# Performance work log

Measured on AMD Instinct MI355X. Metric: run time of the kernel, lower is better.

Reference implementation:

```python
import jax, jax.numpy as jnp
import numpy as np

N = 8192      # number of tree nodes
IN = 1024     # in_dim
M = 1024      # effective mem_dim = 2 * mem_dim_init
K = 8         # max children (complete 8-ary tree)


def _linear_init(key, out_dim, in_dim):
    k1, k2 = jax.random.split(key)
    s = 1.0 / np.sqrt(in_dim)
    w = jax.random.uniform(k1, (out_dim, in_dim), minval=-s, maxval=s, dtype=jnp.float32)
    b = jax.random.uniform(k2, (out_dim,), minval=-s, maxval=s, dtype=jnp.float32)
    return w, b


def setup_inputs() -> dict:
    key = jax.random.key(0)
    ks = jax.random.split(key, 5)
    w_ioux, b_ioux = _linear_init(ks[0], 3 * M, IN)
    w_iouh, b_iouh = _linear_init(ks[1], 3 * M, M)
    w_fx, b_fx = _linear_init(ks[2], M, IN)
    w_fh, b_fh = _linear_init(ks[3], M, M)
    inputs = jax.random.normal(ks[4], (N, IN), dtype=jnp.float32)
    # Complete K-ary tree: children of node p are p*K+1 .. p*K+K (clipped).
    # Pad with index N, which addresses an always-zero dummy row.
    ch = np.full((N, K), N, dtype=np.int32)
    for j in range(K):
        idx = np.arange(N) * K + 1 + j
        valid = idx < N
        ch[valid, j] = idx[valid]
    return dict(inputs=inputs, children=jnp.asarray(ch),
                w_ioux=w_ioux, b_ioux=b_ioux, w_iouh=w_iouh, b_iouh=b_iouh,
                w_fx=w_fx, b_fx=b_fx, w_fh=w_fh, b_fh=b_fh)


def reference(inputs, children, w_ioux, b_ioux, w_iouh, b_iouh, w_fx, b_fx, w_fh, b_fh):
    # Precompute the input-side projections for all nodes at once.
    iou_x = inputs @ w_ioux.T + b_ioux   # [N, 3M]
    fx_x = inputs @ w_fx.T + b_fx        # [N, M]
    h0 = jnp.zeros((N + 1, M), inputs.dtype)  # row N is the zero pad slot
    c0 = jnp.zeros((N + 1, M), inputs.dtype)

    def step(carry, t):
        h_buf, c_buf = carry
        ch = children[t]           # [K] child indices (pad = N -> zero rows)
        ch_h = h_buf[ch]           # [K, M] real child h's
        ch_c = c_buf[ch]           # [K, M] real child c's
        # Faithful to original: for internal nodes child_c/child_h are SWAPPED,
        # so the 'child_h_sum' and f-gate inputs use the real c's, while the
        # forgotten memory (fc) multiplies the real h's. Leaves: all zeros.
        csum = ch_c.sum(0)                                   # [M]
        iou = iou_x[t] + csum @ w_iouh.T + b_iouh            # [3M]
        i_g, o_g, u_g = jnp.split(iou, 3)
        i_g = jax.nn.sigmoid(i_g)
        o_g = jax.nn.sigmoid(o_g)
        u_g = jnp.tanh(u_g)
        f = jax.nn.sigmoid(ch_c @ w_fh.T + b_fh + fx_x[t])   # [K, M]
        c = i_g * u_g + (f * ch_h).sum(0)                    # [M]
        h = o_g * jnp.tanh(c)
        return (h_buf.at[t].set(h), c_buf.at[t].set(c)), None

    # Children always have larger indices than their parent, so processing
    # t = N-1 .. 0 matches the original reverse-BFS (leaves-first) order.
    order = jnp.arange(N - 1, -1, -1)
    (h_buf, c_buf), _ = jax.lax.scan(step, (h0, c0), order)
    root_h = h_buf[0][None, :]   # [1, M]
    root_c = c_buf[0][None, :]   # [1, M]
    return root_h, root_c
```

## Files before the change

kernel.cpp:

```cpp
#include <hip/hip_runtime.h>

typedef __bf16 bf16x8 __attribute__((ext_vector_type(8)));
typedef __attribute__((ext_vector_type(4))) float f4;

#define AS1 __attribute__((address_space(1)))
#define AS3 __attribute__((address_space(3)))

__device__ __forceinline__ unsigned short f2bf(float f) {
    union { float f; unsigned int u; } x; x.f = f;
    return (unsigned short)((x.u + 0x7fffu + ((x.u >> 16) & 1u)) >> 16);
}
__device__ __forceinline__ float bf2f(unsigned short u) {
    union { unsigned int u; float f; } x; x.u = (unsigned int)u << 16;
    return x.f;
}
__device__ __forceinline__ float fsigm(float x) {
    return __builtin_amdgcn_rcpf(1.f + __expf(-x));
}
__device__ __forceinline__ float ftanh(float x) {
    return 1.f - 2.f * __builtin_amdgcn_rcpf(1.f + __expf(2.f * x));
}
__device__ __forceinline__ void gload_lds16(const unsigned short* g, unsigned short* l) {
    __builtin_amdgcn_global_load_lds((const AS1 unsigned int*)g, (AS3 unsigned int*)l, 16, 0, 0);
}
__device__ __forceinline__ void bar() {
    asm volatile("" ::: "memory");
    __builtin_amdgcn_s_barrier();
    asm volatile("" ::: "memory");
}

__global__ void prep_all_k(const float* __restrict__ inputs, const float* __restrict__ w_ioux,
                           const float* __restrict__ w_fx, const float* __restrict__ w_iouh,
                           const float* __restrict__ w_fh,
                           const float* __restrict__ b_ioux, const float* __restrict__ b_iouh,
                           const float* __restrict__ b_fx, const float* __restrict__ b_fh,
                           unsigned short* __restrict__ Xbf, unsigned short* __restrict__ Wiouxbf,
                           unsigned short* __restrict__ Wfxbf, unsigned short* __restrict__ Whbf,
                           unsigned short* __restrict__ Wfhbf,
                           float* __restrict__ bias_iou, float* __restrict__ bias_f,
                           unsigned short* __restrict__ c_bf, unsigned short* __restrict__ h_bf) {
    int b = blockIdx.x;
    if (b < 16384) {
        int idx = b * 256 + threadIdx.x;
        const float* src; unsigned short* dst; int rel;
        if (idx < 2097152)      { src = inputs; dst = Xbf;     rel = idx; }
        else if (idx < 2883584) { src = w_ioux; dst = Wiouxbf; rel = idx - 2097152; }
        else if (idx < 3145728) { src = w_fx;   dst = Wfxbf;   rel = idx - 2883584; }
        else if (idx < 3932160) { src = w_iouh; dst = Whbf;    rel = idx - 3145728; }
        else                    { src = w_fh;   dst = Wfhbf;   rel = idx - 3932160; }
        float4 v = reinterpret_cast<const float4*>(src)[rel];
        ushort4 o; o.x = f2bf(v.x); o.y = f2bf(v.y); o.z = f2bf(v.z); o.w = f2bf(v.w);
        reinterpret_cast<ushort4*>(dst)[rel] = o;
    } else if (b < 16400) {
        int idx = (b - 16384) * 256 + threadIdx.x;
        if (idx < 3072) bias_iou[idx] = b_ioux[idx] + b_iouh[idx];
        else { int j = idx - 3072; bias_f[j] = b_fx[j] + b_fh[j]; }
    } else {
        int j = (b - 16400) * 256 + threadIdx.x;
        size_t o = (size_t)8192 * 1024 + j;
        c_bf[o] = 0; h_bf[o] = 0;
    }
}

__device__ __forceinline__ void stage_half(const unsigned short* __restrict__ G,
                                           int trow0, int kt, unsigned short* lds_region, int tid) {
#pragma unroll
    for (int ii = 0; ii < 2; ++ii) {
        int c = ii * 512 + tid;
        int r = c >> 3, sl = c & 7;
        gload_lds16(G + (size_t)(trow0 + r) * 1024 + kt * 64 + ((sl ^ (r & 7)) * 8),
                    lds_region + c * 8);
    }
}
__device__ __forceinline__ bf16x8 rdfrag(const unsigned short* region, int rowih, int kslot) {
    return *reinterpret_cast<const bf16x8*>(&region[rowih * 64 + ((kslot ^ (rowih & 7)) * 8)]);
}

#define RD_A(AF, REG, FB)                                                        \
    _Pragma("unroll") for (int f_ = 0; f_ < 4; ++f_)                             \
    _Pragma("unroll") for (int s_ = 0; s_ < 2; ++s_)                             \
        (AF)[f_][s_] = rdfrag((REG), ((FB) + f_) * 16 + fr, s_ * 4 + q);
#define RD_B(BQ, REG, GB)                                                        \
    _Pragma("unroll") for (int g_ = 0; g_ < 2; ++g_)                             \
    _Pragma("unroll") for (int s_ = 0; s_ < 2; ++s_)                             \
        (BQ)[g_][s_] = rdfrag((REG), bcol0 + ((GB) + g_) * 16 + fr, s_ * 4 + q);
#define MF16(FB, GB, AF, BQ)                                                     \
    __builtin_amdgcn_s_setprio(1);                                               \
    _Pragma("unroll") for (int s_ = 0; s_ < 2; ++s_)                             \
    _Pragma("unroll") for (int f_ = 0; f_ < 4; ++f_)                             \
    _Pragma("unroll") for (int g_ = 0; g_ < 2; ++g_)                             \
        acc[(FB) + f_][(GB) + g_] = __builtin_amdgcn_mfma_f32_16x16x32_bf16(     \
            (AF)[f_][s_], (BQ)[g_][s_], acc[(FB) + f_][(GB) + g_], 0, 0, 0);     \
    __builtin_amdgcn_s_setprio(0);

__device__ __forceinline__ void gemm256_core(const unsigned short* __restrict__ Am,
                                             const unsigned short* __restrict__ Bm,
                                             int tm, int tn,
                                             unsigned short* ls, f4 acc[8][4]) {
    const int tid = threadIdx.x;
    const int l = tid & 63, w = tid >> 6;
    const int wm = w >> 2, wn = w & 3;
    const int fr = l & 15, q = l >> 4;
    const int bcol0 = (wn & 1) * 64;

    unsigned short* S0 = ls;
    unsigned short* S1 = ls + 32768;
    const unsigned short* Ar0 = S0 + wm * 8192;
    const unsigned short* Br0 = S0 + (2 + (wn >> 1)) * 8192;
    const unsigned short* Ar1 = S1 + wm * 8192;
    const unsigned short* Br1 = S1 + (2 + (wn >> 1)) * 8192;

#pragma unroll
    for (int i = 0; i < 8; ++i)
#pragma unroll
        for (int j = 0; j < 4; ++j) acc[i][j] = (f4){0.f, 0.f, 0.f, 0.f};

    stage_half(Am, tm,       0, S0 + 0 * 8192, tid);
    stage_half(Am, tm + 128, 0, S0 + 1 * 8192, tid);
    stage_half(Bm, tn,       0, S0 + 2 * 8192, tid);
    stage_half(Bm, tn + 128, 0, S0 + 3 * 8192, tid);
    stage_half(Bm, tn,       1, S1 + 2 * 8192, tid);
    stage_half(Bm, tn + 128, 1, S1 + 3 * 8192, tid);
    asm volatile("s_waitcnt vmcnt(4)" ::: "memory");
    bar();

    for (int i = 0; i < 8; ++i) {
        bf16x8 afA[4][2], afB[4][2], bq01[2][2], bq23[2][2];
        RD_A(afA, Ar0, 0)
        RD_B(bq01, Br0, 0)
        stage_half(Am, tm,       2 * i + 1, S1 + 0 * 8192, tid);
        asm volatile("s_waitcnt lgkmcnt(8)" ::: "memory");
        bar();
        MF16(0, 0, afA, bq01)
        bar();
        RD_B(bq23, Br0, 2)
        stage_half(Am, tm + 128, 2 * i + 1, S1 + 1 * 8192, tid);
        bar();
        MF16(0, 2, afA, bq23)
        bar();
        RD_A(afB, Ar0, 4)
        if (i < 7) stage_half(Bm, tn,       2 * i + 2, S0 + 2 * 8192, tid);
        bar();
        MF16(4, 2, afB, bq23)
        bar();
        if (i < 7) {
            stage_half(Bm, tn + 128, 2 * i + 2, S0 + 3 * 8192, tid);
            asm volatile("s_waitcnt vmcnt(4)" ::: "memory");
        } else {
            asm volatile("s_waitcnt vmcnt(0)" ::: "memory");
        }
        bar();
        MF16(4, 0, afB, bq01)
        bar();
        RD_A(afA, Ar1, 0)
        RD_B(bq01, Br1, 0)
        if (i < 7) stage_half(Am, tm,       2 * i + 2, S0 + 0 * 8192, tid);
        asm volatile("s_waitcnt lgkmcnt(8)" ::: "memory");
        bar();
        MF16(0, 0, afA, bq01)
        bar();
        RD_B(bq23, Br1, 2)
        if (i < 7) stage_half(Am, tm + 128, 2 * i + 2, S0 + 1 * 8192, tid);
        bar();
        MF16(0, 2, afA, bq23)
        bar();
        RD_A(afB, Ar1, 4)
        if (i < 7) stage_half(Bm, tn,       2 * i + 3, S1 + 2 * 8192, tid);
        bar();
        MF16(4, 2, afB, bq23)
        bar();
        if (i < 7) {
            stage_half(Bm, tn + 128, 2 * i + 3, S1 + 3 * 8192, tid);
            asm volatile("s_waitcnt vmcnt(4)" ::: "memory");
        } else {
            asm volatile("s_waitcnt vmcnt(0)" ::: "memory");
        }
        bar();
        MF16(4, 0, afB, bq01)
        bar();
    }
}

__global__ __launch_bounds__(512, 2)
void gemm_big_k(const unsigned short* __restrict__ Xbf, const unsigned short* __restrict__ Wioux,
                const unsigned short* __restrict__ Wfx,
                const float* __restrict__ bias_iou, const float* __restrict__ bias_f,
                unsigned short* __restrict__ P_iou, unsigned short* __restrict__ P_f) {
    __shared__ unsigned short ls[65536];
    int b = blockIdx.x;
    b = (b & 7) * 50 + (b >> 3);
    const unsigned short* Bm; unsigned short* Cp; const float* biasp;
    int tm, tn, ldc;
    if (b < 384) {
        int st = b / 24, wt = b % 24;
        tm = ((st >> 2) * 8 + wt / 3) * 256;
        tn = ((st & 3) * 3 + wt % 3) * 256;
        Bm = Wioux; Cp = P_iou; biasp = bias_iou; ldc = 3072;
    } else {
        int bb = b - 384;
        tm = (bb & 3) * 256; tn = (bb >> 2) * 256;
        Bm = Wfx; Cp = P_f; biasp = bias_f; ldc = 1024;
    }
    f4 acc[8][4];
    gemm256_core(Xbf, Bm, tm, tn, ls, acc);

    const int l = threadIdx.x & 63, w = threadIdx.x >> 6;
    const int wm = w >> 2, wn = w & 3;
    const int fr = l & 15, q = l >> 4;
#pragma unroll
    for (int f = 0; f < 8; ++f)
#pragma unroll
        for (int g = 0; g < 4; ++g) {
            int col = tn + wn * 64 + g * 16 + fr;
            float bv = biasp[col];
#pragma unroll
            for (int r = 0; r < 4; ++r) {
                int row = tm + wm * 128 + f * 16 + q * 4 + r;
                Cp[(size_t)row * ldc + col] = f2bf(acc[f][g][r] + bv);
            }
        }
}

__device__ __forceinline__ void gemm_core_db(const unsigned short* __restrict__ A,
                                             const unsigned short* __restrict__ B,
                                             int M, int tile_m, int tile_n, int kb, int nsteps,
                                             unsigned short* lsA, unsigned short* lsB,
                                             f4 acc[4][4]) {
    const int K = 1024;
    const int tid = threadIdx.x;
    const int l = tid & 63, wid = tid >> 6;
    const int wm = wid >> 1, wn = wid & 1;
    const int fr = l & 15, q = l >> 4;

#pragma unroll
    for (int i = 0; i < 4; ++i)
#pragma unroll
        for (int j = 0; j < 4; ++j) acc[i][j] = (f4){0.f, 0.f, 0.f, 0.f};

    const unsigned short* ga[4]; const unsigned short* gb[4];
    unsigned short *la[4], *lb[4];
#pragma unroll
    for (int i = 0; i < 4; ++i) {
        int chunk = i * 256 + tid;
        int row = chunk >> 3, slot = chunk & 7;
        int scol = (slot ^ (row & 7)) * 8;
        ga[i] = A + (size_t)min(tile_m + row, M - 1) * K + kb * 64 + scol;
        gb[i] = B + (size_t)(tile_n + row) * K + kb * 64 + scol;
        la[i] = lsA + chunk * 8;
        lb[i] = lsB + chunk * 8;
    }
#pragma unroll
    for (int i = 0; i < 4; ++i) gload_lds16(ga[i], la[i]);
#pragma unroll
    for (int i = 0; i < 4; ++i) gload_lds16(gb[i], lb[i]);

    int roffA[4], roffB[4];
#pragma unroll
    for (int f = 0; f < 4; ++f) {
        roffA[f] = (wm * 64 + f * 16 + fr) * 64;
        roffB[f] = (wn * 64 + f * 16 + fr) * 64;
    }
    const int sw = fr & 7;
    int cur = 0;
    for (int t = 0; t < nsteps; ++t) {
        if (t < nsteps - 1) {
            int k0 = (t + 1) * 64;
            int nb = (cur ^ 1) * 8192;
#pragma unroll
            for (int i = 0; i < 4; ++i) gload_lds16(ga[i] + k0, la[i] + nb);
#pragma unroll
            for (int i = 0; i < 4; ++i) gload_lds16(gb[i] + k0, lb[i] + nb);
            asm volatile("s_waitcnt vmcnt(8)" ::: "memory");
        } else {
            asm volatile("s_waitcnt vmcnt(0)" ::: "memory");
        }
        __builtin_amdgcn_s_barrier();
        const unsigned short* bA = lsA + cur * 8192;
        const unsigned short* bB = lsB + cur * 8192;
        bf16x8 af[4][2], bq[4][2];
#pragma unroll
        for (int f = 0; f < 4; ++f)
#pragma unroll
            for (int s = 0; s < 2; ++s) {
                int sl = ((s * 4 + q) ^ sw) * 8;
                af[f][s] = *reinterpret_cast<const bf16x8*>(&bA[roffA[f] + sl]);
                bq[f][s] = *reinterpret_cast<const bf16x8*>(&bB[roffB[f] + sl]);
            }
#pragma unroll
        for (int s = 0; s < 2; ++s)
#pragma unroll
            for (int i = 0; i < 4; ++i)
#pragma unroll
                for (int j = 0; j < 4; ++j)
                    acc[i][j] = __builtin_amdgcn_mfma_f32_16x16x32_bf16(af[i][s], bq[j][s], acc[i][j], 0, 0, 0);
        __builtin_amdgcn_s_barrier();
        cur ^= 1;
    }
}

__global__ void leafact_csum_k(const unsigned short* __restrict__ P_iou,
                               unsigned short* __restrict__ h_bf, unsigned short* __restrict__ c_bf,
                               unsigned short* __restrict__ csum_bf) {
    int b = blockIdx.x;
    int j = threadIdx.x * 4;
    if (b < 896) {
        int p = 128 + b;
        float s0 = 0.f, s1 = 0.f, s2 = 0.f, s3 = 0.f;
#pragma unroll
        for (int k = 0; k < 8; ++k) {
            int t = p * 8 + 1 + k;
            const unsigned short* pp = P_iou + (size_t)t * 3072 + j;
            ushort4 pi = *reinterpret_cast<const ushort4*>(pp);
            ushort4 po = *reinterpret_cast<const ushort4*>(pp + 1024);
            ushort4 pu = *reinterpret_cast<const ushort4*>(pp + 2048);
            float c0 = fsigm(bf2f(pi.x)) * ftanh(bf2f(pu.x));
            float c1 = fsigm(bf2f(pi.y)) * ftanh(bf2f(pu.y));
            float c2 = fsigm(bf2f(pi.z)) * ftanh(bf2f(pu.z));
            float c3 = fsigm(bf2f(pi.w)) * ftanh(bf2f(pu.w));
            ushort4 cb, hb;
            cb.x = f2bf(c0); hb.x = f2bf(fsigm(bf2f(po.x)) * ftanh(c0));
            cb.y = f2bf(c1); hb.y = f2bf(fsigm(bf2f(po.y)) * ftanh(c1));
            cb.z = f2bf(c2); hb.z = f2bf(fsigm(bf2f(po.z)) * ftanh(c2));
            cb.w = f2bf(c3); hb.w = f2bf(fsigm(bf2f(po.w)) * ftanh(c3));
            size_t o = (size_t)t * 1024 + j;
            *reinterpret_cast<ushort4*>(c_bf + o) = cb;
            *reinterpret_cast<ushort4*>(h_bf + o) = hb;
            s0 += c0; s1 += c1; s2 += c2; s3 += c3;
        }
        ushort4 sv; sv.x = f2bf(s0); sv.y = f2bf(s1); sv.z = f2bf(s2); sv.w = f2bf(s3);
        *reinterpret_cast<ushort4*>(csum_bf + (size_t)p * 1024 + j) = sv;
    } else {
        const int t = 1024;
        const unsigned short* pp = P_iou + (size_t)t * 3072 + j;
        ushort4 pi = *reinterpret_cast<const ushort4*>(pp);
        ushort4 po = *reinterpret_cast<const ushort4*>(pp + 1024);
        ushort4 pu = *reinterpret_cast<const ushort4*>(pp + 2048);
        float c0 = fsigm(bf2f(pi.x)) * ftanh(bf2f(pu.x));
        float c1 = fsigm(bf2f(pi.y)) * ftanh(bf2f(pu.y));
        float c2 = fsigm(bf2f(pi.z)) * ftanh(bf2f(pu.z));
        float c3 = fsigm(bf2f(pi.w)) * ftanh(bf2f(pu.w));
        ushort4 cb, hb;
        cb.x = f2bf(c0); hb.x = f2bf(fsigm(bf2f(po.x)) * ftanh(c0));
        cb.y = f2bf(c1); hb.y = f2bf(fsigm(bf2f(po.y)) * ftanh(c1));
        cb.z = f2bf(c2); hb.z = f2bf(fsigm(bf2f(po.z)) * ftanh(c2));
        cb.w = f2bf(c3); hb.w = f2bf(fsigm(bf2f(po.w)) * ftanh(c3));
        size_t o = (size_t)t * 1024 + j;
        *reinterpret_cast<ushort4*>(c_bf + o) = cb;
        *reinterpret_cast<ushort4*>(h_bf + o) = hb;
    }
}

__global__ void csum_k(const unsigned short* __restrict__ c_bf, unsigned short* __restrict__ csum_bf,
                       int lo, int n) {
    int w = blockIdx.x * blockDim.x + threadIdx.x;
    if (w >= n * 256) return;
    int tt = w >> 8, j = (w & 255) * 4;
    int t = lo + tt;
    size_t base = (size_t)(t * 8 + 1) * 1024 + j;
    float s0 = 0.f, s1 = 0.f, s2 = 0.f, s3 = 0.f;
#pragma unroll
    for (int k = 0; k < 8; ++k) {
        ushort4 v = *reinterpret_cast<const ushort4*>(c_bf + base + (size_t)k * 1024);
        s0 += bf2f(v.x); s1 += bf2f(v.y); s2 += bf2f(v.z); s3 += bf2f(v.w);
    }
    ushort4 o; o.x = f2bf(s0); o.y = f2bf(s1); o.z = f2bf(s2); o.w = f2bf(s3);
    *reinterpret_cast<ushort4*>(csum_bf + (size_t)t * 1024 + j) = o;
}

__global__ void node_update_k(const unsigned short* __restrict__ P_iou,
                              const unsigned short* __restrict__ P_f,
                              const float* __restrict__ out_iouh, const float* __restrict__ out_f,
                              unsigned short* __restrict__ h_bf, unsigned short* __restrict__ c_bf,
                              float* __restrict__ out, int lo, int n) {
    int w = blockIdx.x * blockDim.x + threadIdx.x;
    if (w >= n * 256) return;
    int tt = w >> 8, j = (w & 255) * 4;
    int t = lo + tt;
    const unsigned short* p = P_iou + (size_t)t * 3072 + j;
    ushort4 pi4 = *reinterpret_cast<const ushort4*>(p);
    ushort4 po4 = *reinterpret_cast<const ushort4*>(p + 1024);
    ushort4 pu4 = *reinterpret_cast<const ushort4*>(p + 2048);
    const float* oi = out_iouh + (size_t)tt * 3072 + j;
    f4 oii = *reinterpret_cast<const f4*>(oi);
    f4 oio = *reinterpret_cast<const f4*>(oi + 1024);
    f4 oiu = *reinterpret_cast<const f4*>(oi + 2048);
    ushort4 pf4 = *reinterpret_cast<const ushort4*>(P_f + (size_t)t * 1024 + j);
    float pf[4] = {bf2f(pf4.x), bf2f(pf4.y), bf2f(pf4.z), bf2f(pf4.w)};
    float a[4], og[4];
    a[0] = fsigm(bf2f(pi4.x) + oii[0]) * ftanh(bf2f(pu4.x) + oiu[0]);
    a[1] = fsigm(bf2f(pi4.y) + oii[1]) * ftanh(bf2f(pu4.y) + oiu[1]);
    a[2] = fsigm(bf2f(pi4.z) + oii[2]) * ftanh(bf2f(pu4.z) + oiu[2]);
    a[3] = fsigm(bf2f(pi4.w) + oii[3]) * ftanh(bf2f(pu4.w) + oiu[3]);
    og[0] = fsigm(bf2f(po4.x) + oio[0]);
    og[1] = fsigm(bf2f(po4.y) + oio[1]);
    og[2] = fsigm(bf2f(po4.z) + oio[2]);
    og[3] = fsigm(bf2f(po4.w) + oio[3]);
#pragma unroll
    for (int k = 0; k < 8; ++k) {
        f4 fo = *reinterpret_cast<const f4*>(out_f + (size_t)(tt * 8 + k) * 1024 + j);
        ushort4 hc = *reinterpret_cast<const ushort4*>(h_bf + (size_t)(t * 8 + 1 + k) * 1024 + j);
        a[0] += fsigm(pf[0] + fo[0]) * bf2f(hc.x);
        a[1] += fsigm(pf[1] + fo[1]) * bf2f(hc.y);
        a[2] += fsigm(pf[2] + fo[2]) * bf2f(hc.z);
        a[3] += fsigm(pf[3] + fo[3]) * bf2f(hc.w);
    }
    float h0 = og[0] * ftanh(a[0]);
    float h1 = og[1] * ftanh(a[1]);
    float h2 = og[2] * ftanh(a[2]);
    float h3 = og[3] * ftanh(a[3]);
    size_t o = (size_t)t * 1024 + j;
    ushort4 cb; cb.x = f2bf(a[0]); cb.y = f2bf(a[1]); cb.z = f2bf(a[2]); cb.w = f2bf(a[3]);
    ushort4 hb; hb.x = f2bf(h0); hb.y = f2bf(h1); hb.z = f2bf(h2); hb.w = f2bf(h3);
    *reinterpret_cast<ushort4*>(c_bf + o) = cb;
    *reinterpret_cast<ushort4*>(h_bf + o) = hb;
    if (t == 0) {
        f4 hv = {h0, h1, h2, h3};
        f4 cv = {a[0], a[1], a[2], a[3]};
        *reinterpret_cast<f4*>(out + j) = hv;
        *reinterpret_cast<f4*>(out + 1024 + j) = cv;
    }
}

struct GDesc {
    const unsigned short* A;
    const unsigned short* B;
    float* C;
    int M;
    int ldc;
    int tiles_n;
    int tiles_total;
};

__global__ __launch_bounds__(256)
void gemm_dual_k(GDesc d0, GDesc d1) {
    __shared__ unsigned short lsA[16384];
    __shared__ unsigned short lsB[16384];
    int b = blockIdx.x;
    GDesc d; int bb;
    if (b < d0.tiles_total) { d = d0; bb = b; }
    else { d = d1; bb = b - d0.tiles_total; }
    const int tile_m = (bb / d.tiles_n) * 128;
    const int tile_n = (bb % d.tiles_n) * 128;
    f4 acc[4][4];
    gemm_core_db(d.A, d.B, d.M, tile_m, tile_n, 0, 16, lsA, lsB, acc);

    const int l = threadIdx.x & 63, wid = threadIdx.x >> 6;
    const int wm = wid >> 1, wn = wid & 1;
    const int fr = l & 15, q = l >> 4;
#pragma unroll
    for (int i = 0; i < 4; ++i)
#pragma unroll
        for (int j = 0; j < 4; ++j) {
            int col = tile_n + wn * 64 + fr + j * 16;
#pragma unroll
            for (int r = 0; r < 4; ++r) {
                int row = tile_m + wm * 64 + q * 4 + i * 16 + r;
                if (row < d.M) d.C[(size_t)row * d.ldc + col] = acc[i][j][r];
            }
        }
}

__global__ __launch_bounds__(256)
void gemm_tail_k(const unsigned short* __restrict__ c_bf,
                 const unsigned short* __restrict__ Whbf, const unsigned short* __restrict__ Wfhbf,
                 float* __restrict__ part_iouh, float* __restrict__ part_f, int lo, int n) {
    __shared__ unsigned short lsA[16384];
    __shared__ unsigned short lsB[16384];
    const int tid = threadIdx.x;
    const int l = tid & 63, wid = tid >> 6;
    const int wm = wid >> 1, wn = wid & 1;
    const int fr = l & 15, q = l >> 4;
    int b = blockIdx.x;
    f4 acc[4][4];
    float* C; int M, ldc, tm, tn;

    if (b < 96) {
        const int split = b & 3, tile = b >> 2;
        M = n; ldc = 3072; tm = 0; tn = tile * 128;
        C = part_iouh + (size_t)split * 64 * 3072;
        for (int e = tid; e < n * 64; e += 256) {
            int r = e >> 6, c4 = e & 63;
            size_t gbase = (size_t)((lo + r) * 8 + 1) * 1024 + split * 256 + c4 * 4;
            float s0 = 0.f, s1 = 0.f, s2 = 0.f, s3 = 0.f;
#pragma unroll
            for (int k = 0; k < 8; ++k) {
                ushort4 v = *reinterpret_cast<const ushort4*>(c_bf + gbase + (size_t)k * 1024);
                s0 += bf2f(v.x); s1 += bf2f(v.y); s2 += bf2f(v.z); s3 += bf2f(v.w);
            }
            ushort4 o; o.x = f2bf(s0); o.y = f2bf(s1); o.z = f2bf(s2); o.w = f2bf(s3);
            int sl8 = c4 >> 1, half = c4 & 1;
            int phys = (sl8 & ~7) | ((sl8 & 7) ^ (r & 7));
            *reinterpret_cast<ushort4*>(&lsA[r * 256 + phys * 8 + half * 4]) = o;
        }
        const unsigned short* gb[4]; unsigned short* lb[4];
#pragma unroll
        for (int i = 0; i < 4; ++i) {
            int chunk = i * 256 + tid;
            int row = chunk >> 3, slot = chunk & 7;
            int scol = (slot ^ (row & 7)) * 8;
            gb[i] = Whbf + (size_t)(tn + row) * 1024 + split * 256 + scol;
            lb[i] = lsB + chunk * 8;
        }
#pragma unroll
        for (int i = 0; i < 4; ++i) gload_lds16(gb[i], lb[i]);
        asm volatile("s_waitcnt lgkmcnt(0)" ::: "memory");
        __builtin_amdgcn_s_barrier();

#pragma unroll
        for (int i2 = 0; i2 < 4; ++i2)
#pragma unroll
            for (int j2 = 0; j2 < 4; ++j2) acc[i2][j2] = (f4){0.f, 0.f, 0.f, 0.f};
        int roffB[4], rA[4];
#pragma unroll
        for (int f = 0; f < 4; ++f) {
            roffB[f] = (wn * 64 + f * 16 + fr) * 64;
            rA[f] = min(wm * 64 + f * 16 + fr, n - 1);
        }
        const int sw = fr & 7;
        int cur = 0;
        for (int t = 0; t < 4; ++t) {
            if (t < 3) {
                int nb = (cur ^ 1) * 8192;
#pragma unroll
                for (int i = 0; i < 4; ++i) gload_lds16(gb[i] + (t + 1) * 64, lb[i] + nb);
                asm volatile("s_waitcnt vmcnt(4)" ::: "memory");
            } else {
                asm volatile("s_waitcnt vmcnt(0)" ::: "memory");
            }
            __builtin_amdgcn_s_barrier();
            const unsigned short* bB = lsB + cur * 8192;
            bf16x8 af[4][2], bq[4][2];
#pragma unroll
            for (int f = 0; f < 4; ++f)
#pragma unroll
                for (int s = 0; s < 2; ++s) {
                    int x = s * 4 + q;
                    af[f][s] = *reinterpret_cast<const bf16x8*>(
                        &lsA[rA[f] * 256 + (t * 8 + (x ^ (rA[f] & 7))) * 8]);
                    bq[f][s] = *reinterpret_cast<const bf16x8*>(&bB[roffB[f] + ((x ^ sw) * 8)]);
                }
// ... 34 lines not shown
                                   const unsigned short* __restrict__ P_f,
                                   const float* __restrict__ part_iouh,
                                   const float* __restrict__ part_f,
                                   unsigned short* __restrict__ h_bf, unsigned short* __restrict__ c_bf,
                                   float* __restrict__ out, int lo, int n) {
    int w = blockIdx.x * blockDim.x + threadIdx.x;
    if (w >= n * 256) return;
    int tt = w >> 8, j = (w & 255) * 4;
    int t = lo + tt;
    f4 oii = {0.f, 0.f, 0.f, 0.f}, oio = oii, oiu = oii;
#pragma unroll
    for (int s = 0; s < 4; ++s) {
        const float* base = part_iouh + (size_t)s * 64 * 3072 + (size_t)tt * 3072 + j;
        oii += *reinterpret_cast<const f4*>(base);
        oio += *reinterpret_cast<const f4*>(base + 1024);
        oiu += *reinterpret_cast<const f4*>(base + 2048);
    }
    const unsigned short* p = P_iou + (size_t)t * 3072 + j;
    ushort4 pi4 = *reinterpret_cast<const ushort4*>(p);
    ushort4 po4 = *reinterpret_cast<const ushort4*>(p + 1024);
    ushort4 pu4 = *reinterpret_cast<const ushort4*>(p + 2048);
    ushort4 pf4 = *reinterpret_cast<const ushort4*>(P_f + (size_t)t * 1024 + j);
    float pf[4] = {bf2f(pf4.x), bf2f(pf4.y), bf2f(pf4.z), bf2f(pf4.w)};
    float a[4], og[4];
    a[0] = fsigm(bf2f(pi4.x) + oii[0]) * ftanh(bf2f(pu4.x) + oiu[0]);
    a[1] = fsigm(bf2f(pi4.y) + oii[1]) * ftanh(bf2f(pu4.y) + oiu[1]);
    a[2] = fsigm(bf2f(pi4.z) + oii[2]) * ftanh(bf2f(pu4.z) + oiu[2]);
    a[3] = fsigm(bf2f(pi4.w) + oii[3]) * ftanh(bf2f(pu4.w) + oiu[3]);
    og[0] = fsigm(bf2f(po4.x) + oio[0]);
    og[1] = fsigm(bf2f(po4.y) + oio[1]);
    og[2] = fsigm(bf2f(po4.z) + oio[2]);
    og[3] = fsigm(bf2f(po4.w) + oio[3]);
#pragma unroll
    for (int k = 0; k < 8; ++k) {
        f4 fo = {0.f, 0.f, 0.f, 0.f};
#pragma unroll
        for (int s = 0; s < 4; ++s)
            fo += *reinterpret_cast<const f4*>(part_f + (size_t)s * 512 * 1024 +
                                               (size_t)(tt * 8 + k) * 1024 + j);
        ushort4 hc = *reinterpret_cast<const ushort4*>(h_bf + (size_t)(t * 8 + 1 + k) * 1024 + j);
        a[0] += fsigm(pf[0] + fo[0]) * bf2f(hc.x);
        a[1] += fsigm(pf[1] + fo[1]) * bf2f(hc.y);
        a[2] += fsigm(pf[2] + fo[2]) * bf2f(hc.z);
        a[3] += fsigm(pf[3] + fo[3]) * bf2f(hc.w);
    }
    float h0 = og[0] * ftanh(a[0]);
    float h1 = og[1] * ftanh(a[1]);
    float h2 = og[2] * ftanh(a[2]);
    float h3 = og[3] * ftanh(a[3]);
    size_t o = (size_t)t * 1024 + j;
    ushort4 cb; cb.x = f2bf(a[0]); cb.y = f2bf(a[1]); cb.z = f2bf(a[2]); cb.w = f2bf(a[3]);
    ushort4 hb; hb.x = f2bf(h0); hb.y = f2bf(h1); hb.z = f2bf(h2); hb.w = f2bf(h3);
    *reinterpret_cast<ushort4*>(c_bf + o) = cb;
    *reinterpret_cast<ushort4*>(h_bf + o) = hb;
    if (t == 0) {
        f4 hv = {h0, h1, h2, h3};
        f4 cv = {a[0], a[1], a[2], a[3]};
        *reinterpret_cast<f4*>(out + j) = hv;
        *reinterpret_cast<f4*>(out + 1024 + j) = cv;
    }
}

extern "C" void kernel_launch(void* const* d_in, const int* in_sizes, int n_in,
                              void* d_out, int out_size, void* d_ws, size_t ws_size,
                              hipStream_t stream) {
    const float* inputs = (const float*)d_in[0];
    const float* w_ioux = (const float*)d_in[2];
    const float* b_ioux = (const float*)d_in[3];
    const float* w_iouh = (const float*)d_in[4];
    const float* b_iouh = (const float*)d_in[5];
    const float* w_fx   = (const float*)d_in[6];
    const float* b_fx   = (const float*)d_in[7];
    const float* w_fh   = (const float*)d_in[8];
    const float* b_fh   = (const float*)d_in[9];
    float* out = (float*)d_out;

    char* ws = (char*)d_ws;
    size_t off = 0;
    auto alloc = [&](size_t bytes) -> void* {
        void* p = ws + off;
        off += (bytes + 255) & ~(size_t)255;
        return p;
    };
    unsigned short* Xbf     = (unsigned short*)alloc((size_t)8192 * 1024 * 2);
    unsigned short* Wiouxbf = (unsigned short*)alloc((size_t)3072 * 1024 * 2);
    unsigned short* Wfxbf   = (unsigned short*)alloc((size_t)1024 * 1024 * 2);
    unsigned short* Whbf    = (unsigned short*)alloc((size_t)3072 * 1024 * 2);
    unsigned short* Wfhbf   = (unsigned short*)alloc((size_t)1024 * 1024 * 2);
    float* bias_iou         = (float*)alloc((size_t)3072 * 4);
    float* bias_f           = (float*)alloc((size_t)1024 * 4);
    unsigned short* P_iou   = (unsigned short*)alloc((size_t)8192 * 3072 * 2);
    unsigned short* P_f     = (unsigned short*)alloc((size_t)1024 * 1024 * 2);
    unsigned short* c_bf    = (unsigned short*)alloc((size_t)8193 * 1024 * 2);
    unsigned short* h_bf    = (unsigned short*)alloc((size_t)8193 * 1024 * 2);
    unsigned short* csum_bf = (unsigned short*)alloc((size_t)1024 * 1024 * 2);
    float* out_iouh         = (float*)alloc((size_t)512 * 3072 * 4);
    float* out_f            = (float*)alloc((size_t)4096 * 1024 * 4);
    float* part_iouh        = (float*)alloc((size_t)4 * 64 * 3072 * 4);
    float* part_f           = (float*)alloc((size_t)4 * 512 * 1024 * 4);

    prep_all_k<<<dim3(16404), dim3(256), 0, stream>>>(
        inputs, w_ioux, w_fx, w_iouh, w_fh, b_ioux, b_iouh, b_fx, b_fh,
        Xbf, Wiouxbf, Wfxbf, Whbf, Wfhbf, bias_iou, bias_f, c_bf, h_bf);

    gemm_big_k<<<dim3(400), dim3(512), 0, stream>>>(Xbf, Wiouxbf, Wfxbf,
                                                    bias_iou, bias_f, P_iou, P_f);
    leafact_csum_k<<<dim3(897), dim3(256), 0, stream>>>(P_iou, h_bf, c_bf, csum_bf);

    {
        const int lo = 585, n = 439;
        GDesc d0, d1;
        d0.A = csum_bf + (size_t)lo * 1024; d0.B = Whbf; d0.C = out_iouh;
        d0.M = n; d0.ldc = 3072; d0.tiles_n = 24;
        d0.tiles_total = ((n + 127) / 128) * 24;
        d1.A = c_bf + (size_t)(lo * 8 + 1) * 1024; d1.B = Wfhbf; d1.C = out_f;
        d1.M = 8 * n; d1.ldc = 1024; d1.tiles_n = 8;
        d1.tiles_total = ((8 * n + 127) / 128) * 8;
        gemm_dual_k<<<dim3(d0.tiles_total + d1.tiles_total), dim3(256), 0, stream>>>(d0, d1);
        node_update_k<<<dim3(n), dim3(256), 0, stream>>>(
            P_iou, P_f, out_iouh, out_f, h_bf, c_bf, out, lo, n);
    }
    {
        const int lo = 73, n = 512;
        csum_k<<<dim3(55), dim3(256), 0, stream>>>(c_bf, csum_bf, 73, 55);
        GDesc d0, d1;
        d0.A = csum_bf + (size_t)lo * 1024; d0.B = Whbf; d0.C = out_iouh;
        d0.M = n; d0.ldc = 3072; d0.tiles_n = 24;
        d0.tiles_total = ((n + 127) / 128) * 24;
        d1.A = c_bf + (size_t)(lo * 8 + 1) * 1024; d1.B = Wfhbf; d1.C = out_f;
        d1.M = 8 * n; d1.ldc = 1024; d1.tiles_n = 8;
        d1.tiles_total = ((8 * n + 127) / 128) * 8;
        gemm_dual_k<<<dim3(d0.tiles_total + d1.tiles_total), dim3(256), 0, stream>>>(d0, d1);
        node_update_k<<<dim3(n), dim3(256), 0, stream>>>(
            P_iou, P_f, out_iouh, out_f, h_bf, c_bf, out, lo, n);
    }
    const int T_LO[3] = {9, 1, 0};
    const int T_N[3]  = {64, 8, 1};
    for (int lv = 0; lv < 3; ++lv) {
        int lo = T_LO[lv], n = T_N[lv];
        int fm_tiles = (8 * n + 127) / 128;
        int nblk = 96 + fm_tiles * 8 * 4;
        gemm_tail_k<<<dim3(nblk), dim3(256), 0, stream>>>(
            c_bf, Whbf, Wfhbf, part_iouh, part_f, lo, n);
        node_update_tail_k<<<dim3(n), dim3(256), 0, stream>>>(
            P_iou, P_f, part_iouh, part_f, h_bf, c_bf, out, lo, n);
    }
    (void)in_sizes; (void)n_in; (void)out_size; (void)ws_size;
}
```

Baseline: 197.4 us.

## Make big input GEMM persistent with cross-tile prefetch of next tile

The input-projection GEMM now launches 256 blocks instead of 400, and the first 144 blocks process a second tile. During the last k-step of the current tile, the prologue loads for the next tile are issued, so the next tile's global loads overlap the current tile's final MFMAs and epilogue. This targets the tail wave left when 400 tiles run on 256 CUs. The cost is some imbalance, since 144 blocks do two tiles while the rest do one, plus slightly more complex control flow.

```diff
diff --git a/kernel.cpp b/kernel.cpp
--- a/kernel.cpp
+++ b/kernel.cpp
@@ -93,10 +93,49 @@
             (AF)[f_][s_], (BQ)[g_][s_], acc[(FB) + f_][(GB) + g_], 0, 0, 0);     \
     __builtin_amdgcn_s_setprio(0);
 
-__device__ __forceinline__ void gemm256_core(const unsigned short* __restrict__ Am,
-                                             const unsigned short* __restrict__ Bm,
-                                             int tm, int tn,
-                                             unsigned short* ls, f4 acc[8][4]) {
+struct TileDesc {
+    const unsigned short* Am;
+    const unsigned short* Bm;
+    unsigned short* Cp;
+    const float* biasp;
+    int tm, tn, ldc;
+};
+
+__device__ __forceinline__ TileDesc resolve_tile(int logical,
+    const unsigned short* Xbf, const unsigned short* Wioux, const unsigned short* Wfx,
+    const float* bias_iou, const float* bias_f,
+    unsigned short* P_iou, unsigned short* P_f) {
+    TileDesc d;
+    int b = (logical & 7) * 50 + (logical >> 3);
+    if (b < 384) {
+        int st = b / 24, wt = b % 24;
+        d.tm = ((st >> 2) * 8 + wt / 3) * 256;
+        d.tn = ((st & 3) * 3 + wt % 3) * 256;
+        d.Am = Xbf; d.Bm = Wioux; d.Cp = P_iou; d.biasp = bias_iou; d.ldc = 3072;
+    } else {
+        int bb = b - 384;
+        d.tm = (bb & 3) * 256; d.tn = (bb >> 2) * 256;
+        d.Am = Xbf; d.Bm = Wfx; d.Cp = P_f; d.biasp = bias_f; d.ldc = 1024;
+    }
+    return d;
+}
+
+__device__ __forceinline__ void stage_prologue(const TileDesc& d,
+                                               unsigned short* S0, unsigned short* S1, int tid) {
+    stage_half(d.Am, d.tm,       0, S0 + 0 * 8192, tid);
+    stage_half(d.Am, d.tm + 128, 0, S0 + 1 * 8192, tid);
+    stage_half(d.Bm, d.tn,       0, S0 + 2 * 8192, tid);
+    stage_half(d.Bm, d.tn + 128, 0, S0 + 3 * 8192, tid);
+    stage_half(d.Bm, d.tn,       1, S1 + 2 * 8192, tid);
+    stage_half(d.Bm, d.tn + 128, 1, S1 + 3 * 8192, tid);
+}
+
+__global__ __launch_bounds__(512, 2)
+void gemm_big_k(const unsigned short* __restrict__ Xbf, const unsigned short* __restrict__ Wioux,
+                const unsigned short* __restrict__ Wfx,
+                const float* __restrict__ bias_iou, const float* __restrict__ bias_f,
+                unsigned short* __restrict__ P_iou, unsigned short* __restrict__ P_f) {
+    __shared__ unsigned short ls[65536];
     const int tid = threadIdx.x;
     const int l = tid & 63, w = tid >> 6;
     const int wm = w >> 2, wn = w & 3;
@@ -110,115 +149,104 @@
     const unsigned short* Ar1 = S1 + wm * 8192;
     const unsigned short* Br1 = S1 + (2 + (wn >> 1)) * 8192;
 
-#pragma unroll
-    for (int i = 0; i < 8; ++i)
-#pragma unroll
-        for (int j = 0; j < 4; ++j) acc[i][j] = (f4){0.f, 0.f, 0.f, 0.f};
-
-    stage_half(Am, tm,       0, S0 + 0 * 8192, tid);
-    stage_half(Am, tm + 128, 0, S0 + 1 * 8192, tid);
-    stage_half(Bm, tn,       0, S0 + 2 * 8192, tid);
-    stage_half(Bm, tn + 128, 0, S0 + 3 * 8192, tid);
-    stage_half(Bm, tn,       1, S1 + 2 * 8192, tid);
-    stage_half(Bm, tn + 128, 1, S1 + 3 * 8192, tid);
-    asm volatile("s_waitcnt vmcnt(4)" ::: "memory");
-    bar();
-
-    for (int i = 0; i < 8; ++i) {
-        bf16x8 afA[4][2], afB[4][2], bq01[2][2], bq23[2][2];
-        RD_A(afA, Ar0, 0)
-        RD_B(bq01, Br0, 0)
-        stage_half(Am, tm,       2 * i + 1, S1 + 0 * 8192, tid);
-        asm volatile("s_waitcnt lgkmcnt(8)" ::: "memory");
+    const int nt = (blockIdx.x < 144) ? 2 : 1;
+    TileDesc cur = resolve_tile(blockIdx.x, Xbf, Wioux, Wfx, bias_iou, bias_f, P_iou, P_f);
+    stage_prologue(cur, S0, S1, tid);
+
+    for (int ti = 0; ti < nt; ++ti) {
+        const bool hn = (ti + 1 < nt);
+        TileDesc nx;
+        if (hn) nx = resolve_tile(blockIdx.x + 256, Xbf, Wioux, Wfx, bias_iou, bias_f, P_iou, P_f);
+
+        asm volatile("s_waitcnt vmcnt(4)" ::: "memory");
         bar();
-        MF16(0, 0, afA, bq01)
-        bar();
-        RD_B(bq23, Br0, 2)
-        stage_half(Am, tm + 128, 2 * i + 1, S1 + 1 * 8192, tid);
-        bar();
-        MF16(0, 2, afA, bq23)
-        bar();
-        RD_A(afB, Ar0, 4)
-        if (i < 7) stage_half(Bm, tn,       2 * i + 2, S0 + 2 * 8192, tid);
-        bar();
-        MF16(4, 2, afB, bq23)
-        bar();
-        if (i < 7) {
-            stage_half(Bm, tn + 128, 2 * i + 2, S0 + 3 * 8192, tid);
-            asm volatile("s_waitcnt vmcnt(4)" ::: "memory");
-        } else {
-            asm volatile("s_waitcnt vmcnt(0)" ::: "memory");
-        }
-        bar();
-        MF16(4, 0, afB, bq01)
-        bar();
-        RD_A(afA, Ar1, 0)
-        RD_B(bq01, Br1, 0)
-        if (i < 7) stage_half(Am, tm,       2 * i + 2, S0 + 0 * 8192, tid);
-        asm volatile("s_waitcnt lgkmcnt(8)" ::: "memory");
-        bar();
-        MF16(0, 0, afA, bq01)
-        bar();
-        RD_B(bq23, Br1, 2)
-        if (i < 7) stage_half(Am, tm + 128, 2 * i + 2, S0 + 1 * 8192, tid);
-        bar();
-        MF16(0, 2, afA, bq23)
-        bar();
-        RD_A(afB, Ar1, 4)
-        if (i < 7) stage_half(Bm, tn,       2 * i + 3, S1 + 2 * 8192, tid);
-        bar();
-        MF16(4, 2, afB, bq23)
-        bar();
-        if (i < 7) {
-            stage_half(Bm, tn + 128, 2 * i + 3, S1 + 3 * 8192, tid);
-            asm volatile("s_waitcnt vmcnt(4)" ::: "memory");
-        } else {
-            asm volatile("s_waitcnt vmcnt(0)" ::: "memory");
-        }
-        bar();
-        MF16(4, 0, afB, bq01)
-        bar();
-    }
-}
-
-__global__ __launch_bounds__(512, 2)
-void gemm_big_k(const unsigned short* __restrict__ Xbf, const unsigned short* __restrict__ Wioux,
-                const unsigned short* __restrict__ Wfx,
-                const float* __restrict__ bias_iou, const float* __restrict__ bias_f,
-                unsigned short* __restrict__ P_iou, unsigned short* __restrict__ P_f) {
-    __shared__ unsigned short ls[65536];
-    int b = blockIdx.x;
-    b = (b & 7) * 50 + (b >> 3);
-    const unsigned short* Bm; unsigned short* Cp; const float* biasp;
-    int tm, tn, ldc;
-    if (b < 384) {
-        int st = b / 24, wt = b % 24;
-        tm = ((st >> 2) * 8 + wt / 3) * 256;
-        tn = ((st & 3) * 3 + wt % 3) * 256;
-        Bm = Wioux; Cp = P_iou; biasp = bias_iou; ldc = 3072;
-    } else {
-        int bb = b - 384;
-        tm = (bb & 3) * 256; tn = (bb >> 2) * 256;
-        Bm = Wfx; Cp = P_f; biasp = bias_f; ldc = 1024;
-    }
-    f4 acc[8][4];
-    gemm256_core(Xbf, Bm, tm, tn, ls, acc);
-
-    const int l = threadIdx.x & 63, w = threadIdx.x >> 6;
-    const int wm = w >> 2, wn = w & 3;
-    const int fr = l & 15, q = l >> 4;
-#pragma unroll
-    for (int f = 0; f < 8; ++f)
-#pragma unroll
-        for (int g = 0; g < 4; ++g) {
-            int col = tn + wn * 64 + g * 16 + fr;
-            float bv = biasp[col];
-#pragma unroll
-            for (int r = 0; r < 4; ++r) {
-                int row = tm + wm * 128 + f * 16 + q * 4 + r;
-                Cp[(size_t)row * ldc + col] = f2bf(acc[f][g][r] + bv);
+
+        f4 acc[8][4];
+#pragma unroll
+        for (int i = 0; i < 8; ++i)
+#pragma unroll
+            for (int j = 0; j < 4; ++j) acc[i][j] = (f4){0.f, 0.f, 0.f, 0.f};
+
+        for (int i = 0; i < 8; ++i) {
+            bf16x8 afA[4][2], afB[4][2], bq01[2][2], bq23[2][2];
+            RD_A(afA, Ar0, 0)
+            RD_B(bq01, Br0, 0)
+            stage_half(cur.Am, cur.tm,       2 * i + 1, S1 + 0 * 8192, tid);
+            asm volatile("s_waitcnt lgkmcnt(8)" ::: "memory");
+            bar();
+            MF16(0, 0, afA, bq01)
+            bar();
+            RD_B(bq23, Br0, 2)
+            stage_half(cur.Am, cur.tm + 128, 2 * i + 1, S1 + 1 * 8192, tid);
+            bar();
+            MF16(0, 2, afA, bq23)
+            bar();
+            RD_A(afB, Ar0, 4)
+            if (i < 7)      stage_half(cur.Bm, cur.tn, 2 * i + 2, S0 + 2 * 8192, tid);
+            else if (hn)    stage_half(nx.Bm,  nx.tn,  0,         S0 + 2 * 8192, tid);
+            bar();
+            MF16(4, 2, afB, bq23)
+            bar();
+            if (i < 7) {
+                stage_half(cur.Bm, cur.tn + 128, 2 * i + 2, S0 + 3 * 8192, tid);
+                asm volatile("s_waitcnt vmcnt(4)" ::: "memory");
+            } else if (hn) {
+                stage_half(nx.Bm, nx.tn + 128, 0, S0 + 3 * 8192, tid);
+                asm volatile("s_waitcnt vmcnt(4)" ::: "memory");
+            } else {
+                asm volatile("s_waitcnt vmcnt(0)" ::: "memory");
             }
-        }
+            bar();
+            MF16(4, 0, afB, bq01)
+            bar();
+            RD_A(afA, Ar1, 0)
+            RD_B(bq01, Br1, 0)
+            if (i < 7)      stage_half(cur.Am, cur.tm, 2 * i + 2, S0 + 0 * 8192, tid);
+            else if (hn)    stage_half(nx.Am,  nx.tm,  0,         S0 + 0 * 8192, tid);
+            asm volatile("s_waitcnt lgkmcnt(8)" ::: "memory");
+            bar();
+            MF16(0, 0, afA, bq01)
+            bar();
+            RD_B(bq23, Br1, 2)
+            if (i < 7)      stage_half(cur.Am, cur.tm + 128, 2 * i + 2, S0 + 1 * 8192, tid);
+            else if (hn)    stage_half(nx.Am,  nx.tm + 128,  0,         S0 + 1 * 8192, tid);
+            bar();
+            MF16(0, 2, afA, bq23)
+            bar();
+            RD_A(afB, Ar1, 4)
+            if (i < 7)      stage_half(cur.Bm, cur.tn, 2 * i + 3, S1 + 2 * 8192, tid);
+            else if (hn)    stage_half(nx.Bm,  nx.tn,  1,         S1 + 2 * 8192, tid);
+            bar();
+            MF16(4, 2, afB, bq23)
+            bar();
+            if (i < 7) {
+                stage_half(cur.Bm, cur.tn + 128, 2 * i + 3, S1 + 3 * 8192, tid);
+                asm volatile("s_waitcnt vmcnt(4)" ::: "memory");
+            } else if (hn) {
+                stage_half(nx.Bm, nx.tn + 128, 1, S1 + 3 * 8192, tid);
+                asm volatile("s_waitcnt vmcnt(4)" ::: "memory");
+            } else {
+                asm volatile("s_waitcnt vmcnt(0)" ::: "memory");
+            }
+            bar();
+            MF16(4, 0, afB, bq01)
+            bar();
+        }
+
+#pragma unroll
+        for (int f = 0; f < 8; ++f)
+#pragma unroll
+            for (int g = 0; g < 4; ++g) {
+                int col = cur.tn + wn * 64 + g * 16 + fr;
+                float bv = cur.biasp[col];
+#pragma unroll
+                for (int r = 0; r < 4; ++r) {
+                    int row = cur.tm + wm * 128 + f * 16 + q * 4 + r;
+                    cur.Cp[(size_t)row * cur.ldc + col] = f2bf(acc[f][g][r] + bv);
+                }
+            }
+        cur = nx;
+    }
 }
 
 __device__ __forceinline__ void gemm_core_db(const unsigned short* __restrict__ A,
@@ -677,7 +705,7 @@
         inputs, w_ioux, w_fx, w_iouh, w_fh, b_ioux, b_iouh, b_fx, b_fh,
         Xbf, Wiouxbf, Wfxbf, Whbf, Wfhbf, bias_iou, bias_f, c_bf, h_bf);
 
-    gemm_big_k<<<dim3(400), dim3(512), 0, stream>>>(Xbf, Wiouxbf, Wfxbf,
+    gemm_big_k<<<dim3(256), dim3(512), 0, stream>>>(Xbf, Wiouxbf, Wfxbf,
                                                     bias_iou, bias_f, P_iou, P_f);
     leafact_csum_k<<<dim3(897), dim3(256), 0, stream>>>(P_iou, h_bf, c_bf, csum_bf);
 
```

Measured after the change: 200.1 us. About the same (+1.4%).

## Batch recurrent GEMMs across tree levels and store intermediates in bf16

Applied to the files above, without the earlier changes.

The first dual GEMM now computes the hidden-side projections for every node whose inputs are already known: parents 128..1023 and all children rows 1025..8192. That leaves the second GEMM only the 55 parents and 440 children that depend on the first node update. GEMM outputs are stored as bf16 in buffers indexed by absolute node row rather than level-relative, which halves intermediate write and read traffic. The leaf kernel also gains a guard so it no longer reads past P_iou or overwrites the zero pad row. In exchange, the first GEMM does more total work up front, and the f and iou pre-activations lose precision from bf16 rounding.

```diff
diff --git a/kernel.cpp b/kernel.cpp
--- a/kernel.cpp
+++ b/kernel.cpp
@@ -309,23 +309,25 @@
 #pragma unroll
         for (int k = 0; k < 8; ++k) {
             int t = p * 8 + 1 + k;
-            const unsigned short* pp = P_iou + (size_t)t * 3072 + j;
-            ushort4 pi = *reinterpret_cast<const ushort4*>(pp);
-            ushort4 po = *reinterpret_cast<const ushort4*>(pp + 1024);
-            ushort4 pu = *reinterpret_cast<const ushort4*>(pp + 2048);
-            float c0 = fsigm(bf2f(pi.x)) * ftanh(bf2f(pu.x));
-            float c1 = fsigm(bf2f(pi.y)) * ftanh(bf2f(pu.y));
-            float c2 = fsigm(bf2f(pi.z)) * ftanh(bf2f(pu.z));
-            float c3 = fsigm(bf2f(pi.w)) * ftanh(bf2f(pu.w));
-            ushort4 cb, hb;
-            cb.x = f2bf(c0); hb.x = f2bf(fsigm(bf2f(po.x)) * ftanh(c0));
-            cb.y = f2bf(c1); hb.y = f2bf(fsigm(bf2f(po.y)) * ftanh(c1));
-            cb.z = f2bf(c2); hb.z = f2bf(fsigm(bf2f(po.z)) * ftanh(c2));
-            cb.w = f2bf(c3); hb.w = f2bf(fsigm(bf2f(po.w)) * ftanh(c3));
-            size_t o = (size_t)t * 1024 + j;
-            *reinterpret_cast<ushort4*>(c_bf + o) = cb;
-            *reinterpret_cast<ushort4*>(h_bf + o) = hb;
-            s0 += c0; s1 += c1; s2 += c2; s3 += c3;
+            if (t < 8192) {
+                const unsigned short* pp = P_iou + (size_t)t * 3072 + j;
+                ushort4 pi = *reinterpret_cast<const ushort4*>(pp);
+                ushort4 po = *reinterpret_cast<const ushort4*>(pp + 1024);
+                ushort4 pu = *reinterpret_cast<const ushort4*>(pp + 2048);
+                float c0 = fsigm(bf2f(pi.x)) * ftanh(bf2f(pu.x));
+                float c1 = fsigm(bf2f(pi.y)) * ftanh(bf2f(pu.y));
+                float c2 = fsigm(bf2f(pi.z)) * ftanh(bf2f(pu.z));
+                float c3 = fsigm(bf2f(pi.w)) * ftanh(bf2f(pu.w));
+                ushort4 cb, hb;
+                cb.x = f2bf(c0); hb.x = f2bf(fsigm(bf2f(po.x)) * ftanh(c0));
+                cb.y = f2bf(c1); hb.y = f2bf(fsigm(bf2f(po.y)) * ftanh(c1));
+                cb.z = f2bf(c2); hb.z = f2bf(fsigm(bf2f(po.z)) * ftanh(c2));
+                cb.w = f2bf(c3); hb.w = f2bf(fsigm(bf2f(po.w)) * ftanh(c3));
+                size_t o = (size_t)t * 1024 + j;
+                *reinterpret_cast<ushort4*>(c_bf + o) = cb;
+                *reinterpret_cast<ushort4*>(h_bf + o) = hb;
+                s0 += c0; s1 += c1; s2 += c2; s3 += c3;
+            }
         }
         ushort4 sv; sv.x = f2bf(s0); sv.y = f2bf(s1); sv.z = f2bf(s2); sv.w = f2bf(s3);
         *reinterpret_cast<ushort4*>(csum_bf + (size_t)p * 1024 + j) = sv;
@@ -369,7 +371,8 @@
 
 __global__ void node_update_k(const unsigned short* __restrict__ P_iou,
                               const unsigned short* __restrict__ P_f,
-                              const float* __restrict__ out_iouh, const float* __restrict__ out_f,
+                              const unsigned short* __restrict__ out_iouh,
+                              const unsigned short* __restrict__ out_f,
                               unsigned short* __restrict__ h_bf, unsigned short* __restrict__ c_bf,
                               float* __restrict__ out, int lo, int n) {
     int w = blockIdx.x * blockDim.x + threadIdx.x;
@@ -380,29 +383,30 @@
     ushort4 pi4 = *reinterpret_cast<const ushort4*>(p);
     ushort4 po4 = *reinterpret_cast<const ushort4*>(p + 1024);
     ushort4 pu4 = *reinterpret_cast<const ushort4*>(p + 2048);
-    const float* oi = out_iouh + (size_t)tt * 3072 + j;
-    f4 oii = *reinterpret_cast<const f4*>(oi);
-    f4 oio = *reinterpret_cast<const f4*>(oi + 1024);
-    f4 oiu = *reinterpret_cast<const f4*>(oi + 2048);
+    const unsigned short* oi = out_iouh + (size_t)t * 3072 + j;
+    ushort4 oii4 = *reinterpret_cast<const ushort4*>(oi);
+    ushort4 oio4 = *reinterpret_cast<const ushort4*>(oi + 1024);
+    ushort4 oiu4 = *reinterpret_cast<const ushort4*>(oi + 2048);
     ushort4 pf4 = *reinterpret_cast<const ushort4*>(P_f + (size_t)t * 1024 + j);
     float pf[4] = {bf2f(pf4.x), bf2f(pf4.y), bf2f(pf4.z), bf2f(pf4.w)};
     float a[4], og[4];
-    a[0] = fsigm(bf2f(pi4.x) + oii[0]) * ftanh(bf2f(pu4.x) + oiu[0]);
-    a[1] = fsigm(bf2f(pi4.y) + oii[1]) * ftanh(bf2f(pu4.y) + oiu[1]);
-    a[2] = fsigm(bf2f(pi4.z) + oii[2]) * ftanh(bf2f(pu4.z) + oiu[2]);
-    a[3] = fsigm(bf2f(pi4.w) + oii[3]) * ftanh(bf2f(pu4.w) + oiu[3]);
-    og[0] = fsigm(bf2f(po4.x) + oio[0]);
-    og[1] = fsigm(bf2f(po4.y) + oio[1]);
-    og[2] = fsigm(bf2f(po4.z) + oio[2]);
-    og[3] = fsigm(bf2f(po4.w) + oio[3]);
+    a[0] = fsigm(bf2f(pi4.x) + bf2f(oii4.x)) * ftanh(bf2f(pu4.x) + bf2f(oiu4.x));
+    a[1] = fsigm(bf2f(pi4.y) + bf2f(oii4.y)) * ftanh(bf2f(pu4.y) + bf2f(oiu4.y));
+    a[2] = fsigm(bf2f(pi4.z) + bf2f(oii4.z)) * ftanh(bf2f(pu4.z) + bf2f(oiu4.z));
+    a[3] = fsigm(bf2f(pi4.w) + bf2f(oii4.w)) * ftanh(bf2f(pu4.w) + bf2f(oiu4.w));
+    og[0] = fsigm(bf2f(po4.x) + bf2f(oio4.x));
+    og[1] = fsigm(bf2f(po4.y) + bf2f(oio4.y));
+    og[2] = fsigm(bf2f(po4.z) + bf2f(oio4.z));
+    og[3] = fsigm(bf2f(po4.w) + bf2f(oio4.w));
 #pragma unroll
     for (int k = 0; k < 8; ++k) {
-        f4 fo = *reinterpret_cast<const f4*>(out_f + (size_t)(tt * 8 + k) * 1024 + j);
-        ushort4 hc = *reinterpret_cast<const ushort4*>(h_bf + (size_t)(t * 8 + 1 + k) * 1024 + j);
-        a[0] += fsigm(pf[0] + fo[0]) * bf2f(hc.x);
-        a[1] += fsigm(pf[1] + fo[1]) * bf2f(hc.y);
-        a[2] += fsigm(pf[2] + fo[2]) * bf2f(hc.z);
-        a[3] += fsigm(pf[3] + fo[3]) * bf2f(hc.w);
+        size_t crow = (size_t)(t * 8 + 1 + k) * 1024 + j;
+        ushort4 fo = *reinterpret_cast<const ushort4*>(out_f + crow);
+        ushort4 hc = *reinterpret_cast<const ushort4*>(h_bf + crow);
+        a[0] += fsigm(pf[0] + bf2f(fo.x)) * bf2f(hc.x);
+        a[1] += fsigm(pf[1] + bf2f(fo.y)) * bf2f(hc.y);
+        a[2] += fsigm(pf[2] + bf2f(fo.z)) * bf2f(hc.z);
+        a[3] += fsigm(pf[3] + bf2f(fo.w)) * bf2f(hc.w);
     }
     float h0 = og[0] * ftanh(a[0]);
     float h1 = og[1] * ftanh(a[1]);
@@ -424,7 +428,7 @@
 struct GDesc {
     const unsigned short* A;
     const unsigned short* B;
-    float* C;
+    unsigned short* C;
     int M;
     int ldc;
     int tiles_n;
@@ -455,7 +459,7 @@
 #pragma unroll
             for (int r = 0; r < 4; ++r) {
                 int row = tile_m + wm * 64 + q * 4 + i * 16 + r;
-                if (row < d.M) d.C[(size_t)row * d.ldc + col] = acc[i][j][r];
+                if (row < d.M) d.C[(size_t)row * d.ldc + col] = f2bf(acc[i][j][r]);
             }
         }
 }
@@ -656,22 +660,22 @@
         off += (bytes + 255) & ~(size_t)255;
         return p;
     };
-    unsigned short* Xbf     = (unsigned short*)alloc((size_t)8192 * 1024 * 2);
-    unsigned short* Wiouxbf = (unsigned short*)alloc((size_t)3072 * 1024 * 2);
-    unsigned short* Wfxbf   = (unsigned short*)alloc((size_t)1024 * 1024 * 2);
-    unsigned short* Whbf    = (unsigned short*)alloc((size_t)3072 * 1024 * 2);
-    unsigned short* Wfhbf   = (unsigned short*)alloc((size_t)1024 * 1024 * 2);
-    float* bias_iou         = (float*)alloc((size_t)3072 * 4);
-    float* bias_f           = (float*)alloc((size_t)1024 * 4);
-    unsigned short* P_iou   = (unsigned short*)alloc((size_t)8192 * 3072 * 2);
-    unsigned short* P_f     = (unsigned short*)alloc((size_t)1024 * 1024 * 2);
-    unsigned short* c_bf    = (unsigned short*)alloc((size_t)8193 * 1024 * 2);
-    unsigned short* h_bf    = (unsigned short*)alloc((size_t)8193 * 1024 * 2);
-    unsigned short* csum_bf = (unsigned short*)alloc((size_t)1024 * 1024 * 2);
-    float* out_iouh         = (float*)alloc((size_t)512 * 3072 * 4);
-    float* out_f            = (float*)alloc((size_t)4096 * 1024 * 4);
-    float* part_iouh        = (float*)alloc((size_t)4 * 64 * 3072 * 4);
-    float* part_f           = (float*)alloc((size_t)4 * 512 * 1024 * 4);
+    unsigned short* Xbf      = (unsigned short*)alloc((size_t)8192 * 1024 * 2);
+    unsigned short* Wiouxbf  = (unsigned short*)alloc((size_t)3072 * 1024 * 2);
+    unsigned short* Wfxbf    = (unsigned short*)alloc((size_t)1024 * 1024 * 2);
+    unsigned short* Whbf     = (unsigned short*)alloc((size_t)3072 * 1024 * 2);
+    unsigned short* Wfhbf    = (unsigned short*)alloc((size_t)1024 * 1024 * 2);
+    float* bias_iou          = (float*)alloc((size_t)3072 * 4);
+    float* bias_f            = (float*)alloc((size_t)1024 * 4);
+    unsigned short* P_iou    = (unsigned short*)alloc((size_t)8192 * 3072 * 2);
+    unsigned short* P_f      = (unsigned short*)alloc((size_t)1024 * 1024 * 2);
+    unsigned short* c_bf     = (unsigned short*)alloc((size_t)8193 * 1024 * 2);
+    unsigned short* h_bf     = (unsigned short*)alloc((size_t)8193 * 1024 * 2);
+    unsigned short* csum_bf  = (unsigned short*)alloc((size_t)1024 * 1024 * 2);
+    unsigned short* out_iouh = (unsigned short*)alloc((size_t)1024 * 3072 * 2);
+    unsigned short* out_f    = (unsigned short*)alloc((size_t)8193 * 1024 * 2);
+    float* part_iouh         = (float*)alloc((size_t)4 * 64 * 3072 * 4);
+    float* part_f            = (float*)alloc((size_t)4 * 512 * 1024 * 4);
 
     prep_all_k<<<dim3(16404), dim3(256), 0, stream>>>(
         inputs, w_ioux, w_fx, w_iouh, w_fh, b_ioux, b_iouh, b_fx, b_fh,
@@ -682,32 +686,32 @@
     leafact_csum_k<<<dim3(897), dim3(256), 0, stream>>>(P_iou, h_bf, c_bf, csum_bf);
 
     {
-        const int lo = 585, n = 439;
         GDesc d0, d1;
-        d0.A = csum_bf + (size_t)lo * 1024; d0.B = Whbf; d0.C = out_iouh;
-        d0.M = n; d0.ldc = 3072; d0.tiles_n = 24;
-        d0.tiles_total = ((n + 127) / 128) * 24;
-        d1.A = c_bf + (size_t)(lo * 8 + 1) * 1024; d1.B = Wfhbf; d1.C = out_f;
-        d1.M = 8 * n; d1.ldc = 1024; d1.tiles_n = 8;
-        d1.tiles_total = ((8 * n + 127) / 128) * 8;
-        gemm_dual_k<<<dim3(d0.tiles_total + d1.tiles_total), dim3(256), 0, stream>>>(d0, d1);
-        node_update_k<<<dim3(n), dim3(256), 0, stream>>>(
-            P_iou, P_f, out_iouh, out_f, h_bf, c_bf, out, lo, n);
-    }
+        d0.A = csum_bf + (size_t)128 * 1024; d0.B = Whbf;
+        d0.C = out_iouh + (size_t)128 * 3072;
+        d0.M = 896; d0.ldc = 3072; d0.tiles_n = 24; d0.tiles_total = 7 * 24;
+        d1.A = c_bf + (size_t)1025 * 1024; d1.B = Wfhbf;
+        d1.C = out_f + (size_t)1025 * 1024;
+        d1.M = 7168; d1.ldc = 1024; d1.tiles_n = 8; d1.tiles_total = 56 * 8;
+        gemm_dual_k<<<dim3(168 + 448), dim3(256), 0, stream>>>(d0, d1);
+    }
+    node_update_k<<<dim3(439), dim3(256), 0, stream>>>(
+        P_iou, P_f, out_iouh, out_f, h_bf, c_bf, out, 585, 439);
+
+    csum_k<<<dim3(55), dim3(256), 0, stream>>>(c_bf, csum_bf, 73, 55);
     {
-        const int lo = 73, n = 512;
-        csum_k<<<dim3(55), dim3(256), 0, stream>>>(c_bf, csum_bf, 73, 55);
         GDesc d0, d1;
-        d0.A = csum_bf + (size_t)lo * 1024; d0.B = Whbf; d0.C = out_iouh;
-        d0.M = n; d0.ldc = 3072; d0.tiles_n = 24;
-        d0.tiles_total = ((n + 127) / 128) * 24;
-        d1.A = c_bf + (size_t)(lo * 8 + 1) * 1024; d1.B = Wfhbf; d1.C = out_f;
-        d1.M = 8 * n; d1.ldc = 1024; d1.tiles_n = 8;
-        d1.tiles_total = ((8 * n + 127) / 128) * 8;
-        gemm_dual_k<<<dim3(d0.tiles_total + d1.tiles_total), dim3(256), 0, stream>>>(d0, d1);
-        node_update_k<<<dim3(n), dim3(256), 0, stream>>>(
-            P_iou, P_f, out_iouh, out_f, h_bf, c_bf, out, lo, n);
-    }
+        d0.A = csum_bf + (size_t)73 * 1024; d0.B = Whbf;
+        d0.C = out_iouh + (size_t)73 * 3072;
+        d0.M = 55; d0.ldc = 3072; d0.tiles_n = 24; d0.tiles_total = 24;
+        d1.A = c_bf + (size_t)585 * 1024; d1.B = Wfhbf;
+        d1.C = out_f + (size_t)585 * 1024;
+        d1.M = 440; d1.ldc = 1024; d1.tiles_n = 8; d1.tiles_total = 4 * 8;
+        gemm_dual_k<<<dim3(24 + 32), dim3(256), 0, stream>>>(d0, d1);
+    }
+    node_update_k<<<dim3(512), dim3(256), 0, stream>>>(
+        P_iou, P_f, out_iouh, out_f, h_bf, c_bf, out, 73, 512);
+
     const int T_LO[3] = {9, 1, 0};
     const int T_N[3]  = {64, 8, 1};
     for (int lv = 0; lv < 3; ++lv) {
```

After: 209.5 us. 1.06x slower.
